# Performance work log

Hardware: AMD Instinct MI355X
Metric: run time of the kernel (lower is better)

## Reference

```python
import jax, jax.numpy as jnp
import numpy as np

B, C, N, K = 2, 128, 8192, 16
DL = 128  # dim_L; Fourier half-dim = 64; mlp hidden = 32


def setup_inputs() -> dict:
    key = jax.random.key(0)
    ks = jax.random.split(key, 16)
    s = 0.05
    return {
        "x": jax.random.normal(ks[0], (B, C, N, 1), jnp.float32),
        "coords": jax.random.normal(ks[1], (B, N, 4), jnp.float32),
        "idx": jax.random.randint(ks[2], (B, N, K), 0, N, jnp.int64),
        "B_gauss": jax.random.normal(ks[3], (4, DL // 2), jnp.float32),
        "W1": jax.random.normal(ks[4], (DL, DL // 4), jnp.float32) * s,
        "b1": jax.random.normal(ks[5], (DL // 4,), jnp.float32) * s,
        "W2": jax.random.normal(ks[6], (DL // 4, C), jnp.float32) * s,
        "b2": jax.random.normal(ks[7], (C,), jnp.float32) * s,
        "Wq": jax.random.normal(ks[8], (C, C), jnp.float32) * s,
        "bq": jax.random.normal(ks[9], (C,), jnp.float32) * s,
        "Wk": jax.random.normal(ks[10], (C, C), jnp.float32) * s,
        "bk": jax.random.normal(ks[11], (C,), jnp.float32) * s,
        "Wv": jax.random.normal(ks[12], (C, C), jnp.float32) * s,
        "bv": jax.random.normal(ks[13], (C,), jnp.float32) * s,
        "Wo": jax.random.normal(ks[14], (C, C), jnp.float32) * s,
        "bo": jax.random.normal(ks[15], (C,), jnp.float32) * s,
    }


def reference(x, coords, idx, B_gauss, W1, b1, W2, b2, Wq, bq, Wk, bk, Wv, bv, Wo, bo):
    xs = x[..., 0]  # [B, C, N]
    # gather neighbor coords/features via KNN idx (vmapped over batch)
    nb_coords = jax.vmap(lambda c, i: c[i])(coords, idx)          # [B, N, K, 4]
    nb_feats = jax.vmap(lambda f, i: f[:, i])(xs, idx)            # [B, C, N, K]
    delta_p = nb_coords - coords[:, :, None, :]                   # [B, N, K, 4]
    # random-Fourier geometric embedding
    proj = jnp.matmul(delta_p, B_gauss)                           # [B, N, K, DL/2]
    two_pi = 2.0 * jnp.pi
    E_freq = jnp.concatenate([jnp.sin(two_pi * proj), jnp.cos(two_pi * proj)], axis=-1)
    h = jax.nn.relu(E_freq @ W1 + b1) @ W2 + b2                   # [B, N, K, C]
    E_geo = jnp.transpose(h, (0, 3, 1, 2))                        # [B, C, N, K]
    # 1x1 conv projections == channel matmuls (PyTorch conv weight acts as out<-in)
    Q = jnp.einsum('oc,bcn->bon', Wq, xs) + bq[None, :, None]     # [B, C, N]
    KV_in = nb_feats + E_geo                                      # [B, C, N, K]
    Kt = jnp.einsum('oc,bcnk->bonk', Wk, KV_in) + bk[None, :, None, None]
    Vt = jnp.einsum('oc,bcnk->bonk', Wv, KV_in) + bv[None, :, None, None]
    # local dot-product attention over K neighbors
    attn = jnp.sum(Q[..., None] * Kt, axis=1, keepdims=True) / jnp.sqrt(jnp.float32(C))
    attn = jax.nn.softmax(attn, axis=-1)                          # [B, 1, N, K]
    out = jnp.sum(attn * Vt, axis=-1, keepdims=True)              # [B, C, N, 1]
    out = jnp.einsum('oc,bcnk->bonk', Wo, out) + bo[None, :, None, None]
    return out
```

## Files before the change

### kernel.cpp

```cpp
#include <hip/hip_runtime.h>


using u16 = unsigned short;
using u32 = unsigned int;
using u64 = unsigned long long;

typedef short bf16x8 __attribute__((ext_vector_type(8)));
typedef float f32x4  __attribute__((ext_vector_type(4)));

__device__ __forceinline__ float bl(u32 u) { return __uint_as_float(u << 16); }
__device__ __forceinline__ float bh(u32 u) { return __uint_as_float(u & 0xffff0000u); }
__device__ __forceinline__ float b2f(u16 u) { return __uint_as_float(((u32)u) << 16); }
__device__ __forceinline__ u16 f2b(float f) {
    u32 u = __float_as_uint(f);
    u32 r = u + 0x7fffu + ((u >> 16) & 1u);
    return (u16)(r >> 16);
}
__device__ __forceinline__ float dot8(uint4 wv, const float* xp) {
    float4 a = *(const float4*)xp;
    float4 b = *(const float4*)(xp + 4);
    return bl(wv.x)*a.x + bh(wv.x)*a.y + bl(wv.y)*a.z + bh(wv.y)*a.w
         + bl(wv.z)*b.x + bh(wv.z)*b.y + bl(wv.w)*b.z + bh(wv.w)*b.w;
}
__device__ __forceinline__ u64 pack4(float a, float b, float c, float d) {
    return (u64)f2b(a) | ((u64)f2b(b) << 16) | ((u64)f2b(c) << 32) | ((u64)f2b(d) << 48);
}
__device__ __forceinline__ int fidxA(int m, int c) {
    return (((m >> 4)*4 + (c >> 5))*64 + ((c >> 3) & 3)*16 + (m & 15))*8 + (c & 7);
}

__global__ void __launch_bounds__(512)
k_pt(const float* __restrict__ x,
     const float* __restrict__ Wq, const float* __restrict__ bq,
     const float* __restrict__ Wk, const float* __restrict__ bk,
     const float* __restrict__ Wv, const float* __restrict__ bv,
     const float* __restrict__ Wo, const float* __restrict__ bo,
     const float* __restrict__ W1, const float* __restrict__ W2,
     u16* __restrict__ Afrag, u16* __restrict__ Wovfrag,
     u16* __restrict__ W1frag, u16* __restrict__ W2frag,
     u16* __restrict__ W2Tfrag,
     float* __restrict__ bA, float* __restrict__ su,
     float* __restrict__ bov, float* __restrict__ d0,
     u16* __restrict__ xT)
{
    const int blk = blockIdx.x, tid = threadIdx.x;

    if (blk >= 130) {
        __shared__ u16 tile[32][33];
        const int blk2 = blk - 130;
        const int b  = blk2 >> 10;
        const int ct = (blk2 >> 8) & 3;
        const int nt = blk2 & 255;
        const int tx = tid & 31, ty = tid >> 5;
        const size_t xb = (size_t)b * 128 * 8192;
        #pragma unroll
        for (int j = 0; j < 2; ++j) {
            int c = ct*32 + ty + j*16;
            tile[ty + j*16][tx] = f2b(x[xb + (size_t)c * 8192 + (size_t)(nt*32 + tx)]);
        }
        __syncthreads();
        #pragma unroll
        for (int j = 0; j < 2; ++j) {
            int n = nt*32 + ty + j*16;
            xT[xb + (size_t)n * 128 + (size_t)(ct*32 + tx)] = tile[tx][ty + j*16];
        }
        return;
    }

    const int i = tid & 127, p = tid >> 7;
    if (blk < 128) {
        __shared__ float sWk[128], sWo[128];
        __shared__ float s_pA[4][128], s_pV[4][128];
        if (tid < 128) sWk[tid] = Wk[tid*128 + blk];
        else if (tid < 256) sWo[tid-128] = Wo[blk*128 + (tid-128)];
        __syncthreads();
        float accA = 0.f, accV = 0.f;
        #pragma unroll 8
        for (int o = p*32; o < p*32 + 32; ++o) {
            accA += sWk[o] * Wq[o*128 + i];
            accV += sWo[o] * Wv[o*128 + i];
        }
        s_pA[p][i] = accA; s_pV[p][i] = accV;
        __syncthreads();
        if (tid < 128) {
            float v = s_pA[0][tid] + s_pA[1][tid] + s_pA[2][tid] + s_pA[3][tid];
            Afrag[fidxA(blk, tid)] = f2b(v);
        } else if (tid < 256) {
            int ii = tid - 128;
            float v = s_pV[0][ii] + s_pV[1][ii] + s_pV[2][ii] + s_pV[3][ii];
            Wovfrag[fidxA(blk, ii)] = f2b(v);
        }
    } else if (blk == 128) {
        __shared__ float s_r[3][4][128];
        float a1 = 0.f, a2 = 0.f, a3 = 0.f;
        #pragma unroll 8
        for (int o = p*32; o < p*32 + 32; ++o) {
            a1 += Wk[o*128 + i] * bq[o];
            a2 += Wq[o*128 + i] * bk[o];
            a3 += Wo[i*128 + o] * bv[o];
        }
        s_r[0][p][i] = a1; s_r[1][p][i] = a2; s_r[2][p][i] = a3;
        __syncthreads();
        if (tid < 128) {
            bA[tid] = s_r[0][0][tid] + s_r[0][1][tid] + s_r[0][2][tid] + s_r[0][3][tid];
        } else if (tid < 256) {
            int ii = tid - 128;
            su[ii] = s_r[1][0][ii] + s_r[1][1][ii] + s_r[1][2][ii] + s_r[1][3][ii];
        } else if (tid < 384) {
            int ii = tid - 256;
            bov[ii] = s_r[2][0][ii] + s_r[2][1][ii] + s_r[2][2][ii] + s_r[2][3][ii] + bo[ii];
        } else if (tid < 448) {
            int l = tid - 384;
            float part = bq[l]*bk[l] + bq[l+64]*bk[l+64];
            part += __shfl_xor(part, 1);
            part += __shfl_xor(part, 2);
            part += __shfl_xor(part, 4);
            part += __shfl_xor(part, 8);
            part += __shfl_xor(part, 16);
            part += __shfl_xor(part, 32);
            if (l == 0) *d0 = part;
        }
    } else {
        for (int e = tid; e < 4096; e += 512) {
            int ii = e & 127, r2 = e >> 7;
            {
                int nt = r2 >> 4, lmm = r2 & 15;
                int ks = ii >> 5, q = (ii >> 3) & 3, j = ii & 7;
                W1frag[((nt*4 + ks)*64 + q*16 + lmm)*8 + j] = f2b(W1[ii*32 + r2]);
            }
            {
                int mt = r2 >> 4, lmm = r2 & 15;
                int ks = ii >> 5, q = (ii >> 3) & 3, j = ii & 7;
                W2frag[((mt*4 + ks)*64 + q*16 + lmm)*8 + j] = f2b(W2[r2*128 + ii]);
            }
            {
                int mt = ii >> 4, lmm = ii & 15;
                int q = r2 >> 3, j = r2 & 7;
                W2Tfrag[(mt*64 + q*16 + lmm)*8 + j] = f2b(W2[r2*128 + ii]);
            }
        }
    }
}

__global__ void __launch_bounds__(256, 4)
k_main(const u16* __restrict__ xT, const float* __restrict__ coords,
       const int* __restrict__ idx, const float* __restrict__ Bg,
       const float* __restrict__ b1g, const float* __restrict__ b2g,
       const u16* __restrict__ Afrag, const u16* __restrict__ Wovfrag,
       const u16* __restrict__ W1frag, const u16* __restrict__ W2frag,
       const u16* __restrict__ W2Tfrag,
       const float* __restrict__ bAg, const float* __restrict__ sug,
       const float* __restrict__ bovg, const float* __restrict__ d0g,
       float* __restrict__ out)
{
    __shared__ __align__(16) u16   sH[128][40];
    __shared__ __align__(16) u16   s_qkb[8][136];
    __shared__ __align__(16) u16   s_gb[8][40];
    __shared__ __align__(16) u16   s_wtb[8][136];
    __shared__ __align__(16) float s_xb[8][132];
    __shared__ __align__(16) float s_del[128][4];
    __shared__ float s_sc[8][17];
    __shared__ float s_attn[8][17];
    __shared__ u16   sHbar[32][12];
    __shared__ float s_e0[8];
    __shared__ __align__(16) float s_b2[128], s_su[128];
    __shared__ float s_bA[128], s_bov[128], s_b1[32];
    __shared__ __align__(16) float sBgT[64][4];
    __shared__ int s_idx[128];

    const int tid = threadIdx.x;
    const int w = tid >> 6, l = tid & 63, lm = l & 15, lq = l >> 4, lmm = lm & 7;
    const int g0 = blockIdx.x * 8;
    const int bsel = g0 >> 13;
    const int n0 = g0 & 8191;
    const size_t bbase = ((size_t)bsel) << 13;
    const float inv_sqrtC = 0.08838834764831845f;

    if (tid < 128) {
        s_bA[tid] = bAg[tid]; s_su[tid] = sug[tid];
        s_bov[tid] = bovg[tid]; s_b2[tid] = b2g[tid];
    } else if (tid < 160) {
        s_b1[tid-128] = b1g[tid-128];
    }
    sBgT[tid >> 2][tid & 3] = Bg[(tid & 3)*64 + (tid >> 2)];
    const float c_d0 = *d0g;

    if (tid < 128) {
        int j = idx[(size_t)g0*16 + tid];
        s_idx[tid] = j;
        float4 cj = *(const float4*)&coords[(size_t)(bbase + j)*4];
        float4 cn = *(const float4*)&coords[(size_t)(g0 + (tid >> 4))*4];
        *(float4*)s_del[tid] = make_float4(cj.x-cn.x, cj.y-cn.y, cj.z-cn.z, cj.w-cn.w);
    }
    f32x4 accq[2] = {{0.f,0.f,0.f,0.f},{0.f,0.f,0.f,0.f}};
    {
        const bf16x8* Af = (const bf16x8*)Afrag;
        bf16x8 bfr[4];
        #pragma unroll
        for (int ks = 0; ks < 4; ++ks)
            bfr[ks] = *(const bf16x8*)&xT[(((size_t)(g0 + lmm)) << 7) + ks*32 + lq*8];
        #pragma unroll
        for (int mi = 0; mi < 2; ++mi) {
            const int ct = w*2 + mi;
            #pragma unroll
            for (int ks = 0; ks < 4; ++ks) {
                bf16x8 a = Af[(ct*4 + ks)*64 + l];
                accq[mi] = __builtin_amdgcn_mfma_f32_16x16x32_bf16(a, bfr[ks], accq[mi], 0, 0, 0);
            }
        }
    }
    __syncthreads();

    if (lm < 8) {
        #pragma unroll
        for (int mi = 0; mi < 2; ++mi) {
            int c0 = (w*2 + mi)*16 + lq*4;
            *(u64*)&s_qkb[lm][c0] = pack4(accq[mi][0] + s_bA[c0],   accq[mi][1] + s_bA[c0+1],
                                          accq[mi][2] + s_bA[c0+2], accq[mi][3] + s_bA[c0+3]);
        }
    }
    __syncthreads();

    {
        const bf16x8* W1f = (const bf16x8*)W1frag;
        bf16x8 w1f[2][4];
        #pragma unroll
        for (int nt = 0; nt < 2; ++nt)
            #pragma unroll
            for (int ks = 0; ks < 4; ++ks) w1f[nt][ks] = W1f[(nt*4 + ks)*64 + l];
        #pragma unroll
        for (int mi = 0; mi < 2; ++mi) {
            const int mt = w*2 + mi;
            float4 d = *(const float4*)s_del[mt*16 + lm];
            bf16x8 ea[4];
            #pragma unroll
            for (int ksp = 0; ksp < 2; ++ksp) {
                #pragma unroll
                for (int jp = 0; jp < 4; ++jp) {
                    int f = ksp*32 + lq*8 + jp*2;
                    float4 ga = *(const float4*)sBgT[f];
                    float4 gb = *(const float4*)sBgT[f+1];
                    float p0 = d.x*ga.x + d.y*ga.y + d.z*ga.z + d.w*ga.w;
                    float p1 = d.x*gb.x + d.y*gb.y + d.z*gb.z + d.w*gb.w;
                    p0 -= floorf(p0); p1 -= floorf(p1);
                    ((u32*)&ea[ksp])[jp]   = (u32)f2b(__builtin_amdgcn_sinf(p0))
                                           | ((u32)f2b(__builtin_amdgcn_sinf(p1)) << 16);
                    ((u32*)&ea[ksp+2])[jp] = (u32)f2b(__builtin_amdgcn_cosf(p0))
                                           | ((u32)f2b(__builtin_amdgcn_cosf(p1)) << 16);
                }
            }
            f32x4 acch[2] = {{0.f,0.f,0.f,0.f},{0.f,0.f,0.f,0.f}};
            #pragma unroll
            for (int ks = 0; ks < 4; ++ks) {
                acch[0] = __builtin_amdgcn_mfma_f32_16x16x32_bf16(ea[ks], w1f[0][ks], acch[0], 0,0,0);
                acch[1] = __builtin_amdgcn_mfma_f32_16x16x32_bf16(ea[ks], w1f[1][ks], acch[1], 0,0,0);
            }
            #pragma unroll
            for (int nt = 0; nt < 2; ++nt) {
                float b1v = s_b1[nt*16 + lm];
                #pragma unroll
                for (int r = 0; r < 4; ++r)
                    sH[mt*16 + lq*4 + r][nt*16 + lm] = f2b(fmaxf(acch[nt][r] + b1v, 0.f));
            }
        }
    }
    if (w < 2) {
        const bf16x8* W2f = (const bf16x8*)W2frag;
        f32x4 accg = {0.f,0.f,0.f,0.f};
        #pragma unroll
        for (int ks = 0; ks < 4; ++ks) {
            bf16x8 a = W2f[(w*4 + ks)*64 + l];
            bf16x8 bv = *(const bf16x8*)&s_qkb[lmm][ks*32 + lq*8];
            accg = __builtin_amdgcn_mfma_f32_16x16x32_bf16(a, bv, accg, 0, 0, 0);
        }
        if (lm < 8) {
            int m0 = w*16 + lq*4;
            *(u64*)&s_gb[lm][m0] = pack4(accg[0], accg[1], accg[2], accg[3]);
        }
    } else {
        int t = tid - 128;
        if (t < 64) {
            int n = t >> 3, sub = t & 7, c0 = sub*16;
            uint4 q0 = *(const uint4*)&s_qkb[n][c0];
            uint4 q1 = *(const uint4*)&s_qkb[n][c0+8];
            uint4 x0 = *(const uint4*)&xT[(((size_t)(g0 + n)) << 7) + c0];
            uint4 x1 = *(const uint4*)&xT[(((size_t)(g0 + n)) << 7) + c0 + 8];
            float part = dot8(q0, &s_b2[c0]) + dot8(q1, &s_b2[c0+8])
                       + dot8(x0, &s_su[c0]) + dot8(x1, &s_su[c0+8]);
            part += __shfl_xor(part, 1);
            part += __shfl_xor(part, 2);
            part += __shfl_xor(part, 4);
            if (sub == 0) s_e0[n] = part + c_d0;
        }
    }
    __syncthreads();

    {
        bf16x8 bq4[5];
        #pragma unroll
        for (int ks = 0; ks < 4; ++ks) bq4[ks] = *(const bf16x8*)&s_qkb[lmm][ks*32 + lq*8];
        bq4[4] = *(const bf16x8*)&s_gb[lmm][lq*8];
        #pragma unroll
        for (int mi = 0; mi < 2; ++mi) {
            const int mt = w*2 + mi;
            const size_t rb = ((size_t)(bbase + s_idx[mt*16 + lm])) << 7;
            f32x4 acc = {0.f,0.f,0.f,0.f};
            #pragma unroll
            for (int ks = 0; ks < 4; ++ks) {
                bf16x8 a = *(const bf16x8*)&xT[rb + ks*32 + lq*8];
                acc = __builtin_amdgcn_mfma_f32_16x16x32_bf16(a, bq4[ks], acc, 0, 0, 0);
            }
            {
                bf16x8 a = *(const bf16x8*)&sH[mt*16 + lm][lq*8];
                acc = __builtin_amdgcn_mfma_f32_16x16x32_bf16(a, bq4[4], acc, 0, 0, 0);
            }
            if (lm == mt) {
                #pragma unroll
                for (int r = 0; r < 4; ++r) s_sc[mt][lq*4 + r] = acc[r];
            }
        }
    }
    __syncthreads();

    if (tid < 128) {
        int n = tid >> 4, k = tid & 15;
        float s = (s_sc[n][k] + s_e0[n]) * inv_sqrtC;
        float mx = s;
        mx = fmaxf(mx, __shfl_xor(mx, 1, 16));
        mx = fmaxf(mx, __shfl_xor(mx, 2, 16));
        mx = fmaxf(mx, __shfl_xor(mx, 4, 16));
        mx = fmaxf(mx, __shfl_xor(mx, 8, 16));
        float ex = __expf(s - mx);
        float sm = ex;
        sm += __shfl_xor(sm, 1, 16);
        sm += __shfl_xor(sm, 2, 16);
        sm += __shfl_xor(sm, 4, 16);
        sm += __shfl_xor(sm, 8, 16);
        s_attn[n][k] = ex / sm;
    }
    __syncthreads();

    {
        int n = tid >> 5, cs = tid & 31, c0 = cs*4;
        float a0[16];
        #pragma unroll
        for (int k = 0; k < 16; ++k) a0[k] = s_attn[n][k];
        float4 facc = *(const float4*)&s_b2[c0];
        #pragma unroll
        for (int k = 0; k < 16; ++k) {
            uint2 v = *(const uint2*)&xT[(((size_t)(bbase + s_idx[n*16 + k])) << 7) + c0];
            facc.x += a0[k]*bl(v.x); facc.y += a0[k]*bh(v.x);
            facc.z += a0[k]*bl(v.y); facc.w += a0[k]*bh(v.y);
        }
        *(float4*)&s_xb[n][c0] = facc;
        int m = cs;
        float hacc = 0.f;
        #pragma unroll
        for (int k = 0; k < 16; ++k) hacc += a0[k] * b2f(sH[n*16 + k][m]);
        sHbar[m][n] = f2b(hacc);
    }
    __syncthreads();

    {
        const bf16x8* W2Tf = (const bf16x8*)W2Tfrag;
        bf16x8 bv;
        #pragma unroll
        for (int j = 0; j < 8; ++j) bv[j] = (short)sHbar[lq*8 + j][lmm];
        #pragma unroll
        for (int mi = 0; mi < 2; ++mi) {
            const int mt = w*2 + mi;
            bf16x8 a = W2Tf[mt*64 + l];
            f32x4 accw = {0.f,0.f,0.f,0.f};
            accw = __builtin_amdgcn_mfma_f32_16x16x32_bf16(a, bv, accw, 0, 0, 0);
            if (lm < 8) {
                int c0 = mt*16 + lq*4;
                float4 xb4 = *(const float4*)&s_xb[lm][c0];
                *(u64*)&s_wtb[lm][c0] = pack4(xb4.x + accw[0], xb4.y + accw[1],
                                              xb4.z + accw[2], xb4.w + accw[3]);
            }
        }
    }
    __syncthreads();

    {
        const bf16x8* Wvf = (const bf16x8*)Wovfrag;
        bf16x8 bv[4];
        #pragma unroll
        for (int ks = 0; ks < 4; ++ks) bv[ks] = *(const bf16x8*)&s_wtb[lmm][ks*32 + lq*8];
        #pragma unroll
        for (int mi = 0; mi < 2; ++mi) {
            const int ct = w*2 + mi;
            f32x4 acco = {0.f,0.f,0.f,0.f};
            #pragma unroll
            for (int ks = 0; ks < 4; ++ks) {
                bf16x8 a = Wvf[(ct*4 + ks)*64 + l];
                acco = __builtin_amdgcn_mfma_f32_16x16x32_bf16(a, bv[ks], acco, 0, 0, 0);
            }
            if (lm < 8) {
                #pragma unroll
                for (int r = 0; r < 4; ++r) {
                    int o = ct*16 + lq*4 + r;
                    out[(((size_t)(bsel*128 + o)) << 13) + n0 + lm] = acco[r] + s_bov[o];
                }
            }
        }
    }
}

extern "C" void kernel_launch(void* const* d_in, const int* in_sizes, int n_in,
                              void* d_out, int out_size, void* d_ws, size_t ws_size,
                              hipStream_t stream)
{
    const float* x      = (const float*)d_in[0];
    const float* coords = (const float*)d_in[1];
    const int*   idx    = (const int*)d_in[2];
    const float* Bg     = (const float*)d_in[3];
    const float* W1     = (const float*)d_in[4];
    const float* b1     = (const float*)d_in[5];
    const float* W2     = (const float*)d_in[6];
    const float* b2     = (const float*)d_in[7];
    const float* Wq     = (const float*)d_in[8];
    const float* bq     = (const float*)d_in[9];
    const float* Wk     = (const float*)d_in[10];
    const float* bk     = (const float*)d_in[11];
    const float* Wv     = (const float*)d_in[12];
    const float* bv     = (const float*)d_in[13];
    const float* Wo     = (const float*)d_in[14];
    const float* bo     = (const float*)d_in[15];
    float* out = (float*)d_out;

    char* ws = (char*)d_ws;
    u16*   Afrag   = (u16*)(ws);
    u16*   Wovfrag = (u16*)(ws + 32768);
    u16*   W1frag  = (u16*)(ws + 65536);
    u16*   W2frag  = (u16*)(ws + 73728);
    u16*   W2Tfrag = (u16*)(ws + 81920);
    float* bA      = (float*)(ws + 90112);
    float* su      = (float*)(ws + 90624);
    float* bov     = (float*)(ws + 91136);
    float* d0      = (float*)(ws + 91648);
    u16*   xT      = (u16*)(ws + 94208);

    k_pt<<<2178, 512, 0, stream>>>(x, Wq, bq, Wk, bk, Wv, bv, Wo, bo, W1, W2,
                                   Afrag, Wovfrag, W1frag, W2frag, W2Tfrag,
                                   bA, su, bov, d0, xT);
    k_main<<<2048, 256, 0, stream>>>(xT, coords, idx, Bg, b1, b2,
                                     Afrag, Wovfrag, W1frag, W2frag, W2Tfrag,
                                     bA, su, bov, d0, out);
}
```

Before: 128.0 us.

## Drop softmax-invariant score terms and fold W2 into output projection

```diff
diff --git a/kernel.cpp b/kernel.cpp
--- a/kernel.cpp
+++ b/kernel.cpp
@@ -16,12 +16,6 @@
     u32 r = u + 0x7fffu + ((u >> 16) & 1u);
     return (u16)(r >> 16);
 }
-__device__ __forceinline__ float dot8(uint4 wv, const float* xp) {
-    float4 a = *(const float4*)xp;
-    float4 b = *(const float4*)(xp + 4);
-    return bl(wv.x)*a.x + bh(wv.x)*a.y + bl(wv.y)*a.z + bh(wv.y)*a.w
-         + bl(wv.z)*b.x + bh(wv.z)*b.y + bl(wv.w)*b.z + bh(wv.w)*b.w;
-}
 __device__ __forceinline__ u64 pack4(float a, float b, float c, float d) {
     return (u64)f2b(a) | ((u64)f2b(b) << 16) | ((u64)f2b(c) << 32) | ((u64)f2b(d) << 48);
 }
@@ -32,15 +26,14 @@
 __global__ void __launch_bounds__(512)
 k_pt(const float* __restrict__ x,
      const float* __restrict__ Wq, const float* __restrict__ bq,
-     const float* __restrict__ Wk, const float* __restrict__ bk,
+     const float* __restrict__ Wk,
      const float* __restrict__ Wv, const float* __restrict__ bv,
      const float* __restrict__ Wo, const float* __restrict__ bo,
      const float* __restrict__ W1, const float* __restrict__ W2,
      u16* __restrict__ Afrag, u16* __restrict__ Wovfrag,
      u16* __restrict__ W1frag, u16* __restrict__ W2frag,
-     u16* __restrict__ W2Tfrag,
-     float* __restrict__ bA, float* __restrict__ su,
-     float* __restrict__ bov, float* __restrict__ d0,
+     u16* __restrict__ Wow2frag,
+     float* __restrict__ bA, float* __restrict__ bov,
      u16* __restrict__ xT)
 {
     const int blk = blockIdx.x, tid = threadIdx.x;
@@ -71,6 +64,8 @@
     if (blk < 128) {
         __shared__ float sWk[128], sWo[128];
         __shared__ float s_pA[4][128], s_pV[4][128];
+        __shared__ float sWovRow[128];
+        __shared__ float s_p2[32][17];
         if (tid < 128) sWk[tid] = Wk[tid*128 + blk];
         else if (tid < 256) sWo[tid-128] = Wo[blk*128 + (tid-128)];
         __syncthreads();
@@ -89,36 +84,39 @@
             int ii = tid - 128;
             float v = s_pV[0][ii] + s_pV[1][ii] + s_pV[2][ii] + s_pV[3][ii];
             Wovfrag[fidxA(blk, ii)] = f2b(v);
+            sWovRow[ii] = v;
+        }
+        __syncthreads();
+        {
+            int h = tid >> 4, sub = tid & 15;
+            float a = 0.f;
+            #pragma unroll
+            for (int jj = 0; jj < 8; ++jj)
+                a += sWovRow[sub*8 + jj] * W2[h*128 + sub*8 + jj];
+            s_p2[h][sub] = a;
+        }
+        __syncthreads();
+        if (tid < 32) {
+            float v = 0.f;
+            #pragma unroll
+            for (int s = 0; s < 16; ++s) v += s_p2[tid][s];
+            Wow2frag[(((blk >> 4)*64 + (tid >> 3)*16 + (blk & 15)))*8 + (tid & 7)] = f2b(v);
         }
     } else if (blk == 128) {
-        __shared__ float s_r[3][4][128];
-        float a1 = 0.f, a2 = 0.f, a3 = 0.f;
+        __shared__ float s_r[2][4][128];
+        float a1 = 0.f, a3 = 0.f;
         #pragma unroll 8
         for (int o = p*32; o < p*32 + 32; ++o) {
             a1 += Wk[o*128 + i] * bq[o];
-            a2 += Wq[o*128 + i] * bk[o];
             a3 += Wo[i*128 + o] * bv[o];
         }
-        s_r[0][p][i] = a1; s_r[1][p][i] = a2; s_r[2][p][i] = a3;
+        s_r[0][p][i] = a1; s_r[1][p][i] = a3;
         __syncthreads();
         if (tid < 128) {
             bA[tid] = s_r[0][0][tid] + s_r[0][1][tid] + s_r[0][2][tid] + s_r[0][3][tid];
         } else if (tid < 256) {
             int ii = tid - 128;
-            su[ii] = s_r[1][0][ii] + s_r[1][1][ii] + s_r[1][2][ii] + s_r[1][3][ii];
-        } else if (tid < 384) {
-            int ii = tid - 256;
-            bov[ii] = s_r[2][0][ii] + s_r[2][1][ii] + s_r[2][2][ii] + s_r[2][3][ii] + bo[ii];
-        } else if (tid < 448) {
-            int l = tid - 384;
-            float part = bq[l]*bk[l] + bq[l+64]*bk[l+64];
-            part += __shfl_xor(part, 1);
-            part += __shfl_xor(part, 2);
-            part += __shfl_xor(part, 4);
-            part += __shfl_xor(part, 8);
-            part += __shfl_xor(part, 16);
-            part += __shfl_xor(part, 32);
-            if (l == 0) *d0 = part;
+            bov[ii] = s_r[1][0][ii] + s_r[1][1][ii] + s_r[1][2][ii] + s_r[1][3][ii] + bo[ii];
         }
     } else {
         for (int e = tid; e < 4096; e += 512) {
@@ -133,11 +131,6 @@
                 int ks = ii >> 5, q = (ii >> 3) & 3, j = ii & 7;
                 W2frag[((mt*4 + ks)*64 + q*16 + lmm)*8 + j] = f2b(W2[r2*128 + ii]);
             }
-            {
-                int mt = ii >> 4, lmm = ii & 15;
-                int q = r2 >> 3, j = r2 & 7;
-                W2Tfrag[(mt*64 + q*16 + lmm)*8 + j] = f2b(W2[r2*128 + ii]);
-            }
         }
     }
 }
@@ -148,23 +141,19 @@
        const float* __restrict__ b1g, const float* __restrict__ b2g,
        const u16* __restrict__ Afrag, const u16* __restrict__ Wovfrag,
        const u16* __restrict__ W1frag, const u16* __restrict__ W2frag,
-       const u16* __restrict__ W2Tfrag,
-       const float* __restrict__ bAg, const float* __restrict__ sug,
-       const float* __restrict__ bovg, const float* __restrict__ d0g,
+       const u16* __restrict__ Wow2frag,
+       const float* __restrict__ bAg, const float* __restrict__ bovg,
        float* __restrict__ out)
 {
     __shared__ __align__(16) u16   sH[128][40];
     __shared__ __align__(16) u16   s_qkb[8][136];
     __shared__ __align__(16) u16   s_gb[8][40];
-    __shared__ __align__(16) u16   s_wtb[8][136];
-    __shared__ __align__(16) float s_xb[8][132];
+    __shared__ __align__(16) u16   s_xbb[8][136];
     __shared__ __align__(16) float s_del[128][4];
-    __shared__ float s_sc[8][17];
     __shared__ float s_attn[8][17];
     __shared__ u16   sHbar[32][12];
-    __shared__ float s_e0[8];
-    __shared__ __align__(16) float s_b2[128], s_su[128];
-    __shared__ float s_bA[128], s_bov[128], s_b1[32];
+    __shared__ __align__(16) float s_b2[128];
+    __shared__ float s_bov[128], s_b1[32];
     __shared__ __align__(16) float sBgT[64][4];
     __shared__ int s_idx[128];
 
@@ -176,14 +165,9 @@
     const size_t bbase = ((size_t)bsel) << 13;
     const float inv_sqrtC = 0.08838834764831845f;
 
-    if (tid < 128) {
-        s_bA[tid] = bAg[tid]; s_su[tid] = sug[tid];
-        s_bov[tid] = bovg[tid]; s_b2[tid] = b2g[tid];
-    } else if (tid < 160) {
-        s_b1[tid-128] = b1g[tid-128];
-    }
+    if (tid < 128) { s_bov[tid] = bovg[tid]; s_b2[tid] = b2g[tid]; }
+    else if (tid < 160) { s_b1[tid-128] = b1g[tid-128]; }
     sBgT[tid >> 2][tid & 3] = Bg[(tid & 3)*64 + (tid >> 2)];
-    const float c_d0 = *d0g;
 
     if (tid < 128) {
         int j = idx[(size_t)g0*16 + tid];
@@ -192,8 +176,8 @@
         float4 cn = *(const float4*)&coords[(size_t)(g0 + (tid >> 4))*4];
         *(float4*)s_del[tid] = make_float4(cj.x-cn.x, cj.y-cn.y, cj.z-cn.z, cj.w-cn.w);
     }
-    f32x4 accq[2] = {{0.f,0.f,0.f,0.f},{0.f,0.f,0.f,0.f}};
-    {
+    {
+        f32x4 accq[2] = {{0.f,0.f,0.f,0.f},{0.f,0.f,0.f,0.f}};
         const bf16x8* Af = (const bf16x8*)Afrag;
         bf16x8 bfr[4];
         #pragma unroll
@@ -208,18 +192,25 @@
                 accq[mi] = __builtin_amdgcn_mfma_f32_16x16x32_bf16(a, bfr[ks], accq[mi], 0, 0, 0);
             }
         }
+        if (lm < 8) {
+            #pragma unroll
+            for (int mi = 0; mi < 2; ++mi) {
+                int c0 = (w*2 + mi)*16 + lq*4;
+                float4 ba4 = *(const float4*)&bAg[c0];
+                *(u64*)&s_qkb[lm][c0] = pack4(accq[mi][0] + ba4.x, accq[mi][1] + ba4.y,
+                                              accq[mi][2] + ba4.z, accq[mi][3] + ba4.w);
+            }
+        }
     }
     __syncthreads();
 
-    if (lm < 8) {
-        #pragma unroll
-        for (int mi = 0; mi < 2; ++mi) {
-            int c0 = (w*2 + mi)*16 + lq*4;
-            *(u64*)&s_qkb[lm][c0] = pack4(accq[mi][0] + s_bA[c0],   accq[mi][1] + s_bA[c0+1],
-                                          accq[mi][2] + s_bA[c0+2], accq[mi][3] + s_bA[c0+3]);
-        }
-    }
-    __syncthreads();
+    bf16x8 xnb[2][4];
+    {
+        const size_t rb0 = ((size_t)(bbase + s_idx[(w*2 + 0)*16 + lm])) << 7;
+        #pragma unroll
+        for (int ks = 0; ks < 4; ++ks)
+            xnb[0][ks] = *(const bf16x8*)&xT[rb0 + ks*32 + lq*8];
+    }
 
     {
         const bf16x8* W1f = (const bf16x8*)W1frag;
@@ -264,6 +255,12 @@
             }
         }
     }
+    {
+        const size_t rb1 = ((size_t)(bbase + s_idx[(w*2 + 1)*16 + lm])) << 7;
+        #pragma unroll
+        for (int ks = 0; ks < 4; ++ks)
+            xnb[1][ks] = *(const bf16x8*)&xT[rb1 + ks*32 + lq*8];
+    }
     if (w < 2) {
         const bf16x8* W2f = (const bf16x8*)W2frag;
         f32x4 accg = {0.f,0.f,0.f,0.f};
@@ -277,21 +274,6 @@
             int m0 = w*16 + lq*4;
             *(u64*)&s_gb[lm][m0] = pack4(accg[0], accg[1], accg[2], accg[3]);
         }
-    } else {
-        int t = tid - 128;
-        if (t < 64) {
-            int n = t >> 3, sub = t & 7, c0 = sub*16;
-            uint4 q0 = *(const uint4*)&s_qkb[n][c0];
-            uint4 q1 = *(const uint4*)&s_qkb[n][c0+8];
-            uint4 x0 = *(const uint4*)&xT[(((size_t)(g0 + n)) << 7) + c0];
-            uint4 x1 = *(const uint4*)&xT[(((size_t)(g0 + n)) << 7) + c0 + 8];
-            float part = dot8(q0, &s_b2[c0]) + dot8(q1, &s_b2[c0+8])
-                       + dot8(x0, &s_su[c0]) + dot8(x1, &s_su[c0+8]);
-            part += __shfl_xor(part, 1);
-            part += __shfl_xor(part, 2);
-            part += __shfl_xor(part, 4);
-            if (sub == 0) s_e0[n] = part + c_d0;
-        }
     }
     __syncthreads();
 
@@ -303,40 +285,32 @@
         #pragma unroll
         for (int mi = 0; mi < 2; ++mi) {
             const int mt = w*2 + mi;
-            const size_t rb = ((size_t)(bbase + s_idx[mt*16 + lm])) << 7;
             f32x4 acc = {0.f,0.f,0.f,0.f};
             #pragma unroll
-            for (int ks = 0; ks < 4; ++ks) {
-                bf16x8 a = *(const bf16x8*)&xT[rb + ks*32 + lq*8];
-                acc = __builtin_amdgcn_mfma_f32_16x16x32_bf16(a, bq4[ks], acc, 0, 0, 0);
-            }
+            for (int ks = 0; ks < 4; ++ks)
+                acc = __builtin_amdgcn_mfma_f32_16x16x32_bf16(xnb[mi][ks], bq4[ks], acc, 0, 0, 0);
             {
                 bf16x8 a = *(const bf16x8*)&sH[mt*16 + lm][lq*8];
                 acc = __builtin_amdgcn_mfma_f32_16x16x32_bf16(a, bq4[4], acc, 0, 0, 0);
             }
+            float s0 = acc[0]*inv_sqrtC, s1 = acc[1]*inv_sqrtC;
+            float s2 = acc[2]*inv_sqrtC, s3 = acc[3]*inv_sqrtC;
+            float mx = fmaxf(fmaxf(s0, s1), fmaxf(s2, s3));
+            mx = fmaxf(mx, __shfl_xor(mx, 16));
+            mx = fmaxf(mx, __shfl_xor(mx, 32));
+            float e0 = __expf(s0 - mx), e1 = __expf(s1 - mx);
+            float e2 = __expf(s2 - mx), e3 = __expf(s3 - mx);
+            float sm = (e0 + e1) + (e2 + e3);
+            sm += __shfl_xor(sm, 16);
+            sm += __shfl_xor(sm, 32);
             if (lm == mt) {
-                #pragma unroll
-                for (int r = 0; r < 4; ++r) s_sc[mt][lq*4 + r] = acc[r];
-            }
-        }
-    }
-    __syncthreads();
-
-    if (tid < 128) {
-        int n = tid >> 4, k = tid & 15;
-        float s = (s_sc[n][k] + s_e0[n]) * inv_sqrtC;
-        float mx = s;
-        mx = fmaxf(mx, __shfl_xor(mx, 1, 16));
-        mx = fmaxf(mx, __shfl_xor(mx, 2, 16));
-        mx = fmaxf(mx, __shfl_xor(mx, 4, 16));
-        mx = fmaxf(mx, __shfl_xor(mx, 8, 16));
-        float ex = __expf(s - mx);
-        float sm = ex;
-        sm += __shfl_xor(sm, 1, 16);
-        sm += __shfl_xor(sm, 2, 16);
-        sm += __shfl_xor(sm, 4, 16);
-        sm += __shfl_xor(sm, 8, 16);
-        s_attn[n][k] = ex / sm;
+                float inv = 1.0f / sm;
+                s_attn[mt][lq*4 + 0] = e0*inv;
+                s_attn[mt][lq*4 + 1] = e1*inv;
+                s_attn[mt][lq*4 + 2] = e2*inv;
+                s_attn[mt][lq*4 + 3] = e3*inv;
+            }
+        }
     }
     __syncthreads();
 
@@ -352,7 +326,7 @@
             facc.x += a0[k]*bl(v.x); facc.y += a0[k]*bh(v.x);
             facc.z += a0[k]*bl(v.y); facc.w += a0[k]*bh(v.y);
         }
-        *(float4*)&s_xb[n][c0] = facc;
+        *(u64*)&s_xbb[n][c0] = pack4(facc.x, facc.y, facc.z, facc.w);
         int m = cs;
         float hacc = 0.f;
         #pragma unroll
@@ -362,35 +336,19 @@
     __syncthreads();
 
     {
-        const bf16x8* W2Tf = (const bf16x8*)W2Tfrag;
-        bf16x8 bv;
-        #pragma unroll
-        for (int j = 0; j < 8; ++j) bv[j] = (short)sHbar[lq*8 + j][lmm];
-        #pragma unroll
-        for (int mi = 0; mi < 2; ++mi) {
-            const int mt = w*2 + mi;
-            bf16x8 a = W2Tf[mt*64 + l];
-            f32x4 accw = {0.f,0.f,0.f,0.f};
-            accw = __builtin_amdgcn_mfma_f32_16x16x32_bf16(a, bv, accw, 0, 0, 0);
-            if (lm < 8) {
-                int c0 = mt*16 + lq*4;
-                float4 xb4 = *(const float4*)&s_xb[lm][c0];
-                *(u64*)&s_wtb[lm][c0] = pack4(xb4.x + accw[0], xb4.y + accw[1],
-                                              xb4.z + accw[2], xb4.w + accw[3]);
-            }
-        }
-    }
-    __syncthreads();
-
-    {
         const bf16x8* Wvf = (const bf16x8*)Wovfrag;
+        const bf16x8* W2f = (const bf16x8*)Wow2frag;
         bf16x8 bv[4];
         #pragma unroll
-        for (int ks = 0; ks < 4; ++ks) bv[ks] = *(const bf16x8*)&s_wtb[lmm][ks*32 + lq*8];
+        for (int ks = 0; ks < 4; ++ks) bv[ks] = *(const bf16x8*)&s_xbb[lmm][ks*32 + lq*8];
+        bf16x8 bvh;
+        #pragma unroll
+        for (int j = 0; j < 8; ++j) bvh[j] = (short)sHbar[lq*8 + j][lmm];
         #pragma unroll
         for (int mi = 0; mi < 2; ++mi) {
             const int ct = w*2 + mi;
             f32x4 acco = {0.f,0.f,0.f,0.f};
+            acco = __builtin_amdgcn_mfma_f32_16x16x32_bf16(W2f[ct*64 + l], bvh, acco, 0, 0, 0);
             #pragma unroll
             for (int ks = 0; ks < 4; ++ks) {
                 bf16x8 a = Wvf[(ct*4 + ks)*64 + l];
@@ -428,23 +386,22 @@
     const float* Wo     = (const float*)d_in[14];
     const float* bo     = (const float*)d_in[15];
     float* out = (float*)d_out;
+    (void)bk;
 
     char* ws = (char*)d_ws;
-    u16*   Afrag   = (u16*)(ws);
-    u16*   Wovfrag = (u16*)(ws + 32768);
-    u16*   W1frag  = (u16*)(ws + 65536);
-    u16*   W2frag  = (u16*)(ws + 73728);
-    u16*   W2Tfrag = (u16*)(ws + 81920);
-    float* bA      = (float*)(ws + 90112);
-    float* su      = (float*)(ws + 90624);
-    float* bov     = (float*)(ws + 91136);
-    float* d0      = (float*)(ws + 91648);
-    u16*   xT      = (u16*)(ws + 94208);
-
-    k_pt<<<2178, 512, 0, stream>>>(x, Wq, bq, Wk, bk, Wv, bv, Wo, bo, W1, W2,
-                                   Afrag, Wovfrag, W1frag, W2frag, W2Tfrag,
-                                   bA, su, bov, d0, xT);
+    u16*   Afrag    = (u16*)(ws);
+    u16*   Wovfrag  = (u16*)(ws + 32768);
+    u16*   W1frag   = (u16*)(ws + 65536);
+    u16*   W2frag   = (u16*)(ws + 73728);
+    u16*   Wow2frag = (u16*)(ws + 81920);
+    float* bA       = (float*)(ws + 90112);
+    float* bov      = (float*)(ws + 90624);
+    u16*   xT       = (u16*)(ws + 94208);
+
+    k_pt<<<2178, 512, 0, stream>>>(x, Wq, bq, Wk, Wv, bv, Wo, bo, W1, W2,
+                                   Afrag, Wovfrag, W1frag, W2frag, Wow2frag,
+                                   bA, bov, xT);
     k_main<<<2048, 256, 0, stream>>>(xT, coords, idx, Bg, b1, b2,
-                                     Afrag, Wovfrag, W1frag, W2frag, W2Tfrag,
-                                     bA, su, bov, d0, out);
-}
+                                     Afrag, Wovfrag, W1frag, W2frag, Wow2frag,
+                                     bA, bov, out);
+}
```

Result: slower. 147.4 us (+15.1%).
